# Performance work log

Hardware: AMD Instinct MI355X
Metric: run time of the kernel (lower is better)

Reference implementation:

```python
import jax, jax.numpy as jnp
import numpy as np

B, S, D = 2, 4096, 512
H, DK, DV = 8, 64, 64
LN_EPS = 1e-5
ATTN_EPS = 1e-6


def layer_norm(x, g, b):
    mu = jnp.mean(x, axis=-1, keepdims=True)
    var = jnp.var(x, axis=-1, keepdims=True)
    return (x - mu) * jax.lax.rsqrt(var + LN_EPS) * g + b


def setup_inputs() -> dict:
    key = jax.random.key(0)
    ks = jax.random.split(key, 12)
    s = 1.0 / np.sqrt(D)
    inp = {
        "Q": jax.random.normal(ks[0], (B, S, D), jnp.float32),
        "K": jax.random.normal(ks[1], (B, S, D), jnp.float32),
        "V": jax.random.normal(ks[2], (B, S, D), jnp.float32),
        "W_q": jax.random.normal(ks[3], (D, H * DK), jnp.float32) * s,
        "W_k": jax.random.normal(ks[4], (D, H * DK), jnp.float32) * s,
        "W_v": jax.random.normal(ks[5], (D, H * DV), jnp.float32) * s,
        "W_o": jax.random.normal(ks[6], (H * DV, D), jnp.float32) * s,
        "ln1_g": jnp.ones((D,), jnp.float32),
        "ln1_b": jnp.zeros((D,), jnp.float32),
        "ln2_g": jnp.ones((D,), jnp.float32),
        "ln2_b": jnp.zeros((D,), jnp.float32),
        "w1": jax.random.normal(ks[7], (4 * D, D), jnp.float32) * s,  # torch Linear: (out, in)
        "b1": jnp.zeros((4 * D,), jnp.float32),
        "w2": jax.random.normal(ks[8], (D, 4 * D), jnp.float32) * (1.0 / np.sqrt(4 * D)),
        "b2": jnp.zeros((D,), jnp.float32),
    }
    return inp


def reference(Q, K, V, W_q, W_k, W_v, W_o, ln1_g, ln1_b, ln2_g, ln2_b, w1, b1, w2, b2):
    Qn = layer_norm(Q, ln1_g, ln1_b)
    # project and split heads: [B,S,H,dk] -> [B,H,S,dk]
    q = (Qn @ W_q).reshape(B, S, H, DK).transpose(0, 2, 1, 3)
    k = (K @ W_k).reshape(B, S, H, DK).transpose(0, 2, 1, 3)
    v = (V @ W_v).reshape(B, S, H, DV).transpose(0, 2, 1, 3)
    scores = jnp.einsum("bhqd,bhkd->bhqk", q, k) / (np.sqrt(DK) + ATTN_EPS)
    attn = jax.nn.softmax(scores, axis=-1)  # same as max-subtract softmax
    ctx = jnp.einsum("bhqk,bhkd->bhqd", attn, v)
    ctx = ctx.transpose(0, 2, 1, 3).reshape(B, S, H * DV)
    att_out = ctx @ W_o  # dropout = identity (eval)
    X = Q + att_out
    Xn = layer_norm(X, ln2_g, ln2_b)
    h = jax.nn.gelu(Xn @ w1.T + b1, approximate=False)
    ffn = h @ w2.T + b2
    return X + ffn
```

## Files before the change

kernel.cpp:

```cpp
#include <hip/hip_runtime.h>

typedef unsigned short u16;
typedef __attribute__((ext_vector_type(8))) short short8;
typedef __attribute__((ext_vector_type(4))) float f32x4;
typedef __attribute__((ext_vector_type(16))) float f32x16;
typedef __attribute__((ext_vector_type(4))) unsigned u32x4;

struct __align__(8) us4 { u16 x, y, z, w; };
struct __align__(8) ui2 { unsigned x, y; };

#define CEXP (1.44269504089f / (8.0f + 1e-6f))

__device__ __forceinline__ u16 f2bf(float f) {
  unsigned u = __builtin_bit_cast(unsigned, f);
  unsigned r = (u + 0x7FFFu + ((u >> 16) & 1u)) >> 16;
  return (u16)r;
}

__device__ __forceinline__ unsigned pack_bf2_trunc(float a, float b) {
  return __builtin_amdgcn_perm(__builtin_bit_cast(unsigned, b),
                               __builtin_bit_cast(unsigned, a), 0x07060302u);
}

__device__ __forceinline__ void async_load16(const void* g, void* l) {
  __builtin_amdgcn_global_load_lds((const __attribute__((address_space(1))) void*)g,
                                   (__attribute__((address_space(3))) void*)l, 16, 0, 0);
}

__global__ void prep_weights(const float* __restrict__ Wq, const float* __restrict__ Wk,
                             const float* __restrict__ Wv, const float* __restrict__ Wo,
                             const float* __restrict__ w1, const float* __restrict__ w2,
                             u16* __restrict__ wqkvT, u16* __restrict__ woT,
                             u16* __restrict__ w1b, u16* __restrict__ w2b) {
  const int z = blockIdx.y;
  const int stride = gridDim.x * blockDim.x;
  const int i0 = blockIdx.x * blockDim.x + threadIdx.x;
  if (z < 4) {
    const float* src = z == 0 ? Wq : z == 1 ? Wk : z == 2 ? Wv : Wo;
    u16* dst = z < 3 ? wqkvT + z * 512 * 512 : woT;
    const float scale = (z == 0) ? CEXP : 1.0f;
    for (int i = i0; i < 512 * 512; i += stride) {
      int n = i >> 9, k = i & 511;
      dst[i] = f2bf(src[k * 512 + n] * scale);
    }
  } else {
    const float* src = z == 4 ? w1 : w2;
    u16* dst = z == 4 ? w1b : w2b;
    for (int i = i0; i < 2048 * 512; i += stride) dst[i] = f2bf(src[i]);
  }
}

template <bool KV>
__launch_bounds__(128)
__global__ void ln_cast(const float* __restrict__ X, const float* __restrict__ gw,
                        const float* __restrict__ bw, u16* __restrict__ Y,
                        const float* __restrict__ Kin, const float* __restrict__ Vin,
                        u16* __restrict__ Kb, u16* __restrict__ Vb) {
  const int row = blockIdx.x, t = threadIdx.x;
  const size_t base = (size_t)row * 512;
  float4 x = ((const float4*)(X + base))[t];
  float s = x.x + x.y + x.z + x.w;
  float ss = x.x * x.x + x.y * x.y + x.z * x.z + x.w * x.w;
#pragma unroll
  for (int off = 32; off > 0; off >>= 1) {
    s += __shfl_xor(s, off);
    ss += __shfl_xor(ss, off);
  }
  __shared__ float red[4];
  if ((t & 63) == 0) { red[(t >> 6) * 2] = s; red[(t >> 6) * 2 + 1] = ss; }
  __syncthreads();
  const float tot = red[0] + red[2], tss = red[1] + red[3];
  const float mu = tot * (1.0f / 512.0f);
  const float var = tss * (1.0f / 512.0f) - mu * mu;
  const float rs = rsqrtf(var + 1e-5f);
  float4 g4 = ((const float4*)gw)[t];
  float4 b4 = ((const float4*)bw)[t];
  us4 o;
  o.x = f2bf((x.x - mu) * rs * g4.x + b4.x);
  o.y = f2bf((x.y - mu) * rs * g4.y + b4.y);
  o.z = f2bf((x.z - mu) * rs * g4.z + b4.z);
  o.w = f2bf((x.w - mu) * rs * g4.w + b4.w);
  ((us4*)(Y + base))[t] = o;
  if constexpr (KV) {
    float4 k4 = ((const float4*)(Kin + base))[t];
    float4 v4 = ((const float4*)(Vin + base))[t];
    us4 ko, vo;
    ko.x = f2bf(k4.x); ko.y = f2bf(k4.y); ko.z = f2bf(k4.z); ko.w = f2bf(k4.w);
    vo.x = f2bf(v4.x); vo.y = f2bf(v4.y); vo.z = f2bf(v4.z); vo.w = f2bf(v4.w);
    ((us4*)(Kb + base))[t] = ko;
    ((us4*)(Vb + base))[t] = vo;
  }
}

__launch_bounds__(256, 3)
__global__ void gemm_qkv(const u16* __restrict__ Aq, const u16* __restrict__ Ak,
                         const u16* __restrict__ Av, const u16* __restrict__ Bt,
                         u16* __restrict__ qb, u16* __restrict__ kb, u16* __restrict__ vtb) {
  __shared__ __align__(16) u16 sA[128 * 32];
  __shared__ __align__(16) u16 sB[128 * 32];
  const int tid = threadIdx.x;
  const int wave = tid >> 6, lane = tid & 63;
  const int l15 = lane & 15, quad = lane >> 4;
  const int qsw = (quad ^ ((l15 >> 1) & 3)) * 8;
  const int m0 = blockIdx.x * 128, n0 = blockIdx.y * 128;
  const int sel = n0 >> 9;
  const u16* A = sel == 0 ? Aq : sel == 1 ? Ak : Av;
  const int wm = (wave >> 1) * 64, wn = (wave & 1) * 64;
  const int u0 = wave * 64 + lane, u1 = u0 + 256;
  const int sw0 = ((u0 & 3) ^ ((u0 >> 3) & 3)) * 8;
  const int K = 512;

  const u16* a0 = A + (size_t)(m0 + (u0 >> 2)) * K + sw0;
  const u16* a1 = A + (size_t)(m0 + (u1 >> 2)) * K + sw0;
  const u16* b0 = Bt + (size_t)(n0 + (u0 >> 2)) * K + sw0;
  const u16* b1p = Bt + (size_t)(n0 + (u1 >> 2)) * K + sw0;

  f32x4 acc[4][4] = {};
  for (int k0 = 0; k0 < K; k0 += 32) {
    async_load16(a0 + k0, &sA[wave * 512]);
    async_load16(a1 + k0, &sA[2048 + wave * 512]);
    async_load16(b0 + k0, &sB[wave * 512]);
    async_load16(b1p + k0, &sB[2048 + wave * 512]);
    __syncthreads();
    short8 af[4], bfr[4];
#pragma unroll
    for (int i = 0; i < 4; i++)
      af[i] = *(const short8*)&sA[(wm + i * 16 + l15) * 32 + qsw];
#pragma unroll
    for (int j = 0; j < 4; j++)
      bfr[j] = *(const short8*)&sB[(wn + j * 16 + l15) * 32 + qsw];
#pragma unroll
    for (int i = 0; i < 4; i++)
#pragma unroll
      for (int j = 0; j < 4; j++)
        acc[i][j] = __builtin_amdgcn_mfma_f32_16x16x32_bf16(af[i], bfr[j], acc[i][j], 0, 0, 0);
    __syncthreads();
  }

#pragma unroll
  for (int i = 0; i < 4; i++) {
#pragma unroll
    for (int j = 0; j < 4; j++) {
      const int ocol = ((n0 + wn) & 511) + j * 16 + l15;
      const int row0 = m0 + wm + i * 16 + quad * 4;
      if (sel < 2) {
        u16* C = sel == 0 ? qb : kb;
#pragma unroll
        for (int r = 0; r < 4; r++) C[(size_t)(row0 + r) * 512 + ocol] = f2bf(acc[i][j][r]);
      } else {
        const int b = row0 >> 12, s0 = row0 & 4095;
        const int hh = ocol >> 6, cc = ocol & 63;
        us4 pk;
        pk.x = f2bf(acc[i][j][0]); pk.y = f2bf(acc[i][j][1]);
        pk.z = f2bf(acc[i][j][2]); pk.w = f2bf(acc[i][j][3]);
        *(us4*)&vtb[((size_t)((b * 8 + hh) * 64 + cc) << 12) + s0] = pk;
      }
    }
  }
}

template <int EP, int TN, int LB>
__launch_bounds__(256, LB)
__global__ void gemm_bt(const u16* __restrict__ A, const u16* __restrict__ Bt,
                        int M, int N, int K, void* __restrict__ Cp,
                        const float* __restrict__ bias, const float* __restrict__ res) {
  constexpr int MI = (TN == 128) ? 4 : 2;
  __shared__ __align__(16) u16 sA[128 * 32];
  __shared__ __align__(16) u16 sB[TN * 32];
  const int tid = threadIdx.x;
  const int wave = tid >> 6, lane = tid & 63;
  const int l15 = lane & 15, quad = lane >> 4;
  const int qsw = (quad ^ ((l15 >> 1) & 3)) * 8;
  const int m0 = blockIdx.x * 128, n0 = blockIdx.y * TN;
  const int wm = (TN == 128) ? (wave >> 1) * 64 : wave * 32;
  const int wn = (TN == 128) ? (wave & 1) * 64 : 0;
  const int u0 = wave * 64 + lane, u1 = u0 + 256;
  const int sw0 = ((u0 & 3) ^ ((u0 >> 3) & 3)) * 8;

  const u16* a0 = A + (size_t)(m0 + (u0 >> 2)) * K + sw0;
  const u16* a1 = A + (size_t)(m0 + (u1 >> 2)) * K + sw0;
  const u16* b0 = Bt + (size_t)(n0 + (u0 >> 2)) * K + sw0;

  f32x4 acc[MI][4] = {};
  for (int k0 = 0; k0 < K; k0 += 32) {
    async_load16(a0 + k0, &sA[wave * 512]);
    async_load16(a1 + k0, &sA[2048 + wave * 512]);
    async_load16(b0 + k0, &sB[wave * 512]);
    if constexpr (TN == 128) {
      const u16* b1p = Bt + (size_t)(n0 + (u1 >> 2)) * K + sw0;
      async_load16(b1p + k0, &sB[2048 + wave * 512]);
    }
    __syncthreads();
    short8 af[MI], bfr[4];
#pragma unroll
    for (int i = 0; i < MI; i++)
      af[i] = *(const short8*)&sA[(wm + i * 16 + l15) * 32 + qsw];
#pragma unroll
    for (int j = 0; j < 4; j++)
      bfr[j] = *(const short8*)&sB[(wn + j * 16 + l15) * 32 + qsw];
#pragma unroll
    for (int i = 0; i < MI; i++)
#pragma unroll
      for (int j = 0; j < 4; j++)
        acc[i][j] = __builtin_amdgcn_mfma_f32_16x16x32_bf16(af[i], bfr[j], acc[i][j], 0, 0, 0);
    __syncthreads();
  }

#pragma unroll
  for (int i = 0; i < MI; i++) {
#pragma unroll
    for (int j = 0; j < 4; j++) {
      const int col = n0 + wn + j * 16 + l15;
      const int row0 = m0 + wm + i * 16 + quad * 4;
      if (EP == 2) {
        float* C = (float*)Cp;
#pragma unroll
        for (int r = 0; r < 4; r++) {
          size_t idx = (size_t)(row0 + r) * N + col;
          C[idx] = acc[i][j][r] + res[idx];
        }
      } else if (EP == 3) {
        u16* C = (u16*)Cp;
        const float bv = bias[col];
#pragma unroll
        for (int r = 0; r < 4; r++) {
          float xx = acc[i][j][r] + bv;
          float gl = 0.5f * xx * (1.0f + erff(xx * 0.70710678118f));
          C[(size_t)(row0 + r) * N + col] = f2bf(gl);
        }
      } else {
        float* C = (float*)Cp;
        const float bv = bias[col];
#pragma unroll
        for (int r = 0; r < 4; r++) {
          size_t idx = (size_t)(row0 + r) * N + col;
          C[idx] = acc[i][j][r] + bv + res[idx];
        }
      }
    }
  }
}

__launch_bounds__(512, 2)
__global__ void attn_kernel(const u16* __restrict__ qb, const u16* __restrict__ kb,
                            const u16* __restrict__ vtb, u16* __restrict__ ctx) {
  __shared__ __align__(16) u16 smem[49152];
  const int tid = threadIdx.x;
  const int wave = tid >> 6, lane = tid & 63;
  const int l31 = lane & 31, hi = lane >> 5;
  const int qg = wave & 3, kh = wave >> 2;
  const int bh = blockIdx.y, b = bh >> 3, h = bh & 7;
  const int q0 = blockIdx.x * 256;
  const size_t rb = (size_t)b * 4096;
  const int qrowA = q0 + qg * 64 + l31;
  const int qrowB = qrowA + 32;

  short8 qfA[4], qfB[4];
#pragma unroll
  for (int ks = 0; ks < 4; ks++) {
    qfA[ks] = *(const short8*)&qb[(rb + qrowA) * 512 + h * 64 + ks * 16 + hi * 8];
    qfB[ks] = *(const short8*)&qb[(rb + qrowB) * 512 + h * 64 + ks * 16 + hi * 8];
  }

  const int uk0 = wave * 64 + lane, uk1 = uk0 + 512;
  const int krow0 = uk0 >> 3, ksl0 = (uk0 & 7) ^ (krow0 & 7);
  const int krow1 = uk1 >> 3, ksl1 = (uk1 & 7) ^ (krow1 & 7);
  const u16* kp0 = kb + (rb + krow0) * 512 + h * 64 + ksl0 * 8;
  const u16* kp1 = kb + (rb + krow1) * 512 + h * 64 + ksl1 * 8;
  const int vrow0 = uk0 >> 4, vsl0 = (uk0 & 15) ^ (vrow0 & 7);
  const int vrow1 = uk1 >> 4, vsl1 = (uk1 & 15) ^ (vrow1 & 7);
  const u16* vp0 = vtb + (size_t)(bh * 64 + vrow0) * 4096 + vsl0 * 8;
  const u16* vp1 = vtb + (size_t)(bh * 64 + vrow1) * 4096 + vsl1 * 8;

#define STAGE(bi)                                                   \
  {                                                                 \
    u16* dK = smem + (bi) * 8192;                                   \
    u16* dV = smem + 24576 + (bi) * 8192;                           \
    async_load16(kp0, &dK[(wave * 64) * 8]);                        \
    async_load16(kp1, &dK[(512 + wave * 64) * 8]);                  \
    async_load16(vp0, &dV[(wave * 64) * 8]);                        \
    async_load16(vp1, &dV[(512 + wave * 64) * 8]);                  \
    kp0 += 128 * 512; kp1 += 128 * 512; vp0 += 128; vp1 += 128;     \
  }

  f32x16 ovA[2] = {}, ovB[2] = {};
  float lA = 0.f, lB = 0.f;

  STAGE(0);
  STAGE(1);
  asm volatile("s_waitcnt vmcnt(4)" ::: "memory");
  __syncthreads();

  for (int t = 0; t < 32; t++) {
    const int cur = t % 3;
    if (t < 30) STAGE((t + 2) % 3);
    const u16* K_ = smem + cur * 8192;
    const u16* V_ = smem + 24576 + cur * 8192;
#pragma unroll
    for (int kk2 = 0; kk2 < 2; kk2++) {
      const int kb32 = kh * 2 + kk2;
      f32x16 stA = {}, stB = {};
      __builtin_amdgcn_s_setprio(1);
#pragma unroll
      for (int ks = 0; ks < 4; ks++) {
        const int row = kb32 * 32 + l31;
        const int sl = (ks * 2 + hi) ^ (l31 & 7);
        short8 kf = *(const short8*)&K_[row * 64 + sl * 8];
        stA = __builtin_amdgcn_mfma_f32_32x32x16_bf16(kf, qfA[ks], stA, 0, 0, 0);
        stB = __builtin_amdgcn_mfma_f32_32x32x16_bf16(kf, qfB[ks], stB, 0, 0, 0);
      }
      __builtin_amdgcn_s_setprio(0);
      float pA[16], pB[16];
#pragma unroll
      for (int i = 0; i < 16; i++) pA[i] = __builtin_amdgcn_exp2f(stA[i]);
#pragma unroll
      for (int i = 0; i < 16; i++) pB[i] = __builtin_amdgcn_exp2f(stB[i]);
#pragma unroll
      for (int i = 0; i < 16; i += 4) {
        lA += (pA[i] + pA[i + 1]) + (pA[i + 2] + pA[i + 3]);
        lB += (pB[i] + pB[i + 1]) + (pB[i + 2] + pB[i + 3]);
      }
      unsigned a0 = pack_bf2_trunc(pA[0], pA[1]), a1 = pack_bf2_trunc(pA[2], pA[3]);
      unsigned a2 = pack_bf2_trunc(pA[4], pA[5]), a3 = pack_bf2_trunc(pA[6], pA[7]);
      unsigned a4 = pack_bf2_trunc(pA[8], pA[9]), a5 = pack_bf2_trunc(pA[10], pA[11]);
      unsigned a6 = pack_bf2_trunc(pA[12], pA[13]), a7 = pack_bf2_trunc(pA[14], pA[15]);
      auto ra0 = __builtin_amdgcn_permlane32_swap(a0, a2, false, false);
      auto ra1 = __builtin_amdgcn_permlane32_swap(a1, a3, false, false);
      auto ra2 = __builtin_amdgcn_permlane32_swap(a4, a6, false, false);
      auto ra3 = __builtin_amdgcn_permlane32_swap(a5, a7, false, false);
      u32x4 wa0 = {ra0[0], ra1[0], ra0[1], ra1[1]};
      u32x4 wa1 = {ra2[0], ra3[0], ra2[1], ra3[1]};
      short8 pfA0 = __builtin_bit_cast(short8, wa0);
      short8 pfA1 = __builtin_bit_cast(short8, wa1);
      unsigned b0 = pack_bf2_trunc(pB[0], pB[1]), b1 = pack_bf2_trunc(pB[2], pB[3]);
      unsigned b2 = pack_bf2_trunc(pB[4], pB[5]), b3 = pack_bf2_trunc(pB[6], pB[7]);
      unsigned b4 = pack_bf2_trunc(pB[8], pB[9]), b5 = pack_bf2_trunc(pB[10], pB[11]);
      unsigned b6 = pack_bf2_trunc(pB[12], pB[13]), b7 = pack_bf2_trunc(pB[14], pB[15]);
      auto rb0 = __builtin_amdgcn_permlane32_swap(b0, b2, false, false);
      auto rb1 = __builtin_amdgcn_permlane32_swap(b1, b3, false, false);
      auto rb2 = __builtin_amdgcn_permlane32_swap(b4, b6, false, false);
      auto rb3 = __builtin_amdgcn_permlane32_swap(b5, b7, false, false);
      u32x4 wb0 = {rb0[0], rb1[0], rb0[1], rb1[1]};
      u32x4 wb1 = {rb2[0], rb3[0], rb2[1], rb3[1]};
      short8 pfB0 = __builtin_bit_cast(short8, wb0);
      short8 pfB1 = __builtin_bit_cast(short8, wb1);
      __builtin_amdgcn_s_setprio(1);
#pragma unroll
      for (int vb = 0; vb < 2; vb++) {
        const int row = vb * 32 + l31;
        const int sl0 = (kb32 * 4 + hi) ^ (l31 & 7);
        const int sl1 = (kb32 * 4 + 2 + hi) ^ (l31 & 7);
        short8 vf0 = *(const short8*)&V_[row * 128 + sl0 * 8];
        short8 vf1 = *(const short8*)&V_[row * 128 + sl1 * 8];
        ovA[vb] = __builtin_amdgcn_mfma_f32_32x32x16_bf16(vf0, pfA0, ovA[vb], 0, 0, 0);
        ovA[vb] = __builtin_amdgcn_mfma_f32_32x32x16_bf16(vf1, pfA1, ovA[vb], 0, 0, 0);
        ovB[vb] = __builtin_amdgcn_mfma_f32_32x32x16_bf16(vf0, pfB0, ovB[vb], 0, 0, 0);
        ovB[vb] = __builtin_amdgcn_mfma_f32_32x32x16_bf16(vf1, pfB1, ovB[vb], 0, 0, 0);
      }
      __builtin_amdgcn_s_setprio(0);
    }
    if (t < 31) {
      if (t < 30)
        asm volatile("s_waitcnt vmcnt(4)" ::: "memory");
      else
        asm volatile("s_waitcnt vmcnt(0)" ::: "memory");
      __syncthreads();
    }
  }
#undef STAGE

  float l2A = lA + __shfl_xor(lA, 32);
  float l2B = lB + __shfl_xor(lB, 32);
  __syncthreads();
  float* mrg = (float*)&smem[0];
  float* mrgl = (float*)&smem[32768];
  if (kh == 1) {
#pragma unroll
    for (int vb = 0; vb < 2; vb++)
#pragma unroll
      for (int e = 0; e < 16; e++) {
        mrg[((qg * 2 + 0) * 32 + vb * 16 + e) * 64 + lane] = ovA[vb][e];
        mrg[((qg * 2 + 1) * 32 + vb * 16 + e) * 64 + lane] = ovB[vb][e];
      }
    mrgl[(qg * 2 + 0) * 64 + lane] = l2A;
    mrgl[(qg * 2 + 1) * 64 + lane] = l2B;
  }
  __syncthreads();
  if (kh == 0) {
    const float invA = 1.0f / (l2A + mrgl[(qg * 2 + 0) * 64 + lane]);
    const float invB = 1.0f / (l2B + mrgl[(qg * 2 + 1) * 64 + lane]);
#pragma unroll
    for (int vb = 0; vb < 2; vb++) {
#pragma unroll
      for (int rg = 0; rg < 4; rg++) {
        us4 oA, oB;
        oA.x = f2bf((ovA[vb][rg * 4 + 0] + mrg[((qg * 2 + 0) * 32 + vb * 16 + rg * 4 + 0) * 64 + lane]) * invA);
        oA.y = f2bf((ovA[vb][rg * 4 + 1] + mrg[((qg * 2 + 0) * 32 + vb * 16 + rg * 4 + 1) * 64 + lane]) * invA);
        oA.z = f2bf((ovA[vb][rg * 4 + 2] + mrg[((qg * 2 + 0) * 32 + vb * 16 + rg * 4 + 2) * 64 + lane]) * invA);
        oA.w = f2bf((ovA[vb][rg * 4 + 3] + mrg[((qg * 2 + 0) * 32 + vb * 16 + rg * 4 + 3) * 64 + lane]) * invA);
        *(us4*)&ctx[(rb + qrowA) * 512 + h * 64 + vb * 32 + rg * 8 + hi * 4] = oA;
        oB.x = f2bf((ovB[vb][rg * 4 + 0] + mrg[((qg * 2 + 1) * 32 + vb * 16 + rg * 4 + 0) * 64 + lane]) * invB);
        oB.y = f2bf((ovB[vb][rg * 4 + 1] + mrg[((qg * 2 + 1) * 32 + vb * 16 + rg * 4 + 1) * 64 + lane]) * invB);
        oB.z = f2bf((ovB[vb][rg * 4 + 2] + mrg[((qg * 2 + 1) * 32 + vb * 16 + rg * 4 + 2) * 64 + lane]) * invB);
        oB.w = f2bf((ovB[vb][rg * 4 + 3] + mrg[((qg * 2 + 1) * 32 + vb * 16 + rg * 4 + 3) * 64 + lane]) * invB);
        *(us4*)&ctx[(rb + qrowB) * 512 + h * 64 + vb * 32 + rg * 8 + hi * 4] = oB;
      }
    }
  }
}

extern "C" void kernel_launch(void* const* d_in, const int* in_sizes, int n_in,
                              void* d_out, int out_size, void* d_ws, size_t ws_size,
                              hipStream_t stream) {
  (void)in_sizes; (void)n_in; (void)out_size; (void)ws_size;
  const float* Q = (const float*)d_in[0];
  const float* K = (const float*)d_in[1];
  const float* V = (const float*)d_in[2];
  const float* W_q = (const float*)d_in[3];
  const float* W_k = (const float*)d_in[4];
  const float* W_v = (const float*)d_in[5];
  const float* W_o = (const float*)d_in[6];
  const float* ln1_g = (const float*)d_in[7];
  const float* ln1_b = (const float*)d_in[8];
  const float* ln2_g = (const float*)d_in[9];
  const float* ln2_b = (const float*)d_in[10];
  const float* w1 = (const float*)d_in[11];
  const float* b1 = (const float*)d_in[12];
  const float* w2 = (const float*)d_in[13];
  const float* b2 = (const float*)d_in[14];

  char* w = (char*)d_ws;
  const size_t MB = 1u << 20;
  u16* wqkvT = (u16*)(w);
  u16* woT = (u16*)(w + 3 * MB / 2);
  u16* w1b = (u16*)(w + 2 * MB);
  u16* w2b = (u16*)(w + 4 * MB);
  u16* Qn  = (u16*)(w + 6 * MB);
  u16* Kb  = (u16*)(w + 14 * MB);
  u16* Vb  = (u16*)(w + 22 * MB);
  u16* qb  = (u16*)(w + 30 * MB);
  u16* kb  = (u16*)(w + 38 * MB);
  u16* vtb = (u16*)(w + 46 * MB);
  u16* ctx = (u16*)(w + 54 * MB);
  float* X = (float*)(w + 62 * MB);
  u16* Xn  = (u16*)(w + 6 * MB);
  u16* hb  = (u16*)(w + 14 * MB);

  prep_weights<<<dim3(128, 6), 256, 0, stream>>>(W_q, W_k, W_v, W_o, w1, w2,
                                                 wqkvT, woT, w1b, w2b);
  ln_cast<true><<<8192, 128, 0, stream>>>(Q, ln1_g, ln1_b, Qn, K, V, Kb, Vb);
  gemm_qkv<<<dim3(64, 12), 256, 0, stream>>>(Qn, Kb, Vb, wqkvT, qb, kb, vtb);
  attn_kernel<<<dim3(16, 16), 512, 0, stream>>>(qb, kb, vtb, ctx);
  gemm_bt<2, 64, 3><<<dim3(64, 8), 256, 0, stream>>>(ctx, woT, 8192, 512, 512, X, nullptr, Q);
  ln_cast<false><<<8192, 128, 0, stream>>>(X, ln2_g, ln2_b, Xn, nullptr, nullptr, nullptr, nullptr);
  gemm_bt<3, 128, 3><<<dim3(64, 16), 256, 0, stream>>>(Xn, w1b, 8192, 2048, 512, hb, b1, nullptr);
  gemm_bt<4, 64, 3><<<dim3(64, 8), 256, 0, stream>>>(hb, w2b, 8192, 512, 2048, (float*)d_out, b2, X);
}
```

Baseline: 322.8 us.

## Split attention keys across four waves per query group and double the grid

The attention kernel now uses 128 query rows per block, with 2 query groups × 4 key-split waves instead of 4 × 2. The grid doubles to 512 blocks, with batch-head as the fast grid axis. The K/V pipeline drops from triple to double buffering, which shrinks shared memory and raises the occupancy target to 4 blocks per CU. Each wave handles one 32-key slice per tile, and a two-step shared-memory tree reduction merges the four partial outputs and sums. The goals are more parallelism and occupancy across CUs. The cost is a full vmcnt(0) wait every iteration, which exposes load latency, plus extra reduction traffic and a risk of register pressure under the tighter launch bound.

```diff
diff --git a/kernel.cpp b/kernel.cpp
--- a/kernel.cpp
+++ b/kernel.cpp
@@ -241,16 +241,16 @@
   }
 }
 
-__launch_bounds__(512, 2)
+__launch_bounds__(512, 4)
 __global__ void attn_kernel(const u16* __restrict__ qb, const u16* __restrict__ kb,
                             const u16* __restrict__ vtb, u16* __restrict__ ctx) {
-  __shared__ __align__(16) u16 smem[49152];
+  __shared__ __align__(16) u16 smem[33792];
   const int tid = threadIdx.x;
   const int wave = tid >> 6, lane = tid & 63;
   const int l31 = lane & 31, hi = lane >> 5;
-  const int qg = wave & 3, kh = wave >> 2;
-  const int bh = blockIdx.y, b = bh >> 3, h = bh & 7;
-  const int q0 = blockIdx.x * 256;
+  const int qg = wave >> 2, kh = wave & 3;
+  const int bh = blockIdx.x, b = bh >> 3, h = bh & 7;
+  const int q0 = blockIdx.y * 128;
   const size_t rb = (size_t)b * 4096;
   const int qrowA = q0 + qg * 64 + l31;
   const int qrowB = qrowA + 32;
@@ -275,7 +275,7 @@
 #define STAGE(bi)                                                   \
   {                                                                 \
     u16* dK = smem + (bi) * 8192;                                   \
-    u16* dV = smem + 24576 + (bi) * 8192;                           \
+    u16* dV = smem + 16384 + (bi) * 8192;                           \
     async_load16(kp0, &dK[(wave * 64) * 8]);                        \
     async_load16(kp1, &dK[(512 + wave * 64) * 8]);                  \
     async_load16(vp0, &dV[(wave * 64) * 8]);                        \
@@ -287,93 +287,110 @@
   float lA = 0.f, lB = 0.f;
 
   STAGE(0);
-  STAGE(1);
-  asm volatile("s_waitcnt vmcnt(4)" ::: "memory");
+  asm volatile("s_waitcnt vmcnt(0)" ::: "memory");
   __syncthreads();
 
   for (int t = 0; t < 32; t++) {
-    const int cur = t % 3;
-    if (t < 30) STAGE((t + 2) % 3);
+    const int cur = t & 1;
+    if (t < 31) STAGE(cur ^ 1);
     const u16* K_ = smem + cur * 8192;
-    const u16* V_ = smem + 24576 + cur * 8192;
-#pragma unroll
-    for (int kk2 = 0; kk2 < 2; kk2++) {
-      const int kb32 = kh * 2 + kk2;
-      f32x16 stA = {}, stB = {};
-      __builtin_amdgcn_s_setprio(1);
-#pragma unroll
-      for (int ks = 0; ks < 4; ks++) {
-        const int row = kb32 * 32 + l31;
-        const int sl = (ks * 2 + hi) ^ (l31 & 7);
-        short8 kf = *(const short8*)&K_[row * 64 + sl * 8];
-        stA = __builtin_amdgcn_mfma_f32_32x32x16_bf16(kf, qfA[ks], stA, 0, 0, 0);
-        stB = __builtin_amdgcn_mfma_f32_32x32x16_bf16(kf, qfB[ks], stB, 0, 0, 0);
-      }
-      __builtin_amdgcn_s_setprio(0);
-      float pA[16], pB[16];
-#pragma unroll
-      for (int i = 0; i < 16; i++) pA[i] = __builtin_amdgcn_exp2f(stA[i]);
-#pragma unroll
-      for (int i = 0; i < 16; i++) pB[i] = __builtin_amdgcn_exp2f(stB[i]);
-#pragma unroll
-      for (int i = 0; i < 16; i += 4) {
-        lA += (pA[i] + pA[i + 1]) + (pA[i + 2] + pA[i + 3]);
-        lB += (pB[i] + pB[i + 1]) + (pB[i + 2] + pB[i + 3]);
-      }
-      unsigned a0 = pack_bf2_trunc(pA[0], pA[1]), a1 = pack_bf2_trunc(pA[2], pA[3]);
-      unsigned a2 = pack_bf2_trunc(pA[4], pA[5]), a3 = pack_bf2_trunc(pA[6], pA[7]);
-      unsigned a4 = pack_bf2_trunc(pA[8], pA[9]), a5 = pack_bf2_trunc(pA[10], pA[11]);
-      unsigned a6 = pack_bf2_trunc(pA[12], pA[13]), a7 = pack_bf2_trunc(pA[14], pA[15]);
-      auto ra0 = __builtin_amdgcn_permlane32_swap(a0, a2, false, false);
-      auto ra1 = __builtin_amdgcn_permlane32_swap(a1, a3, false, false);
-      auto ra2 = __builtin_amdgcn_permlane32_swap(a4, a6, false, false);
-      auto ra3 = __builtin_amdgcn_permlane32_swap(a5, a7, false, false);
-      u32x4 wa0 = {ra0[0], ra1[0], ra0[1], ra1[1]};
-      u32x4 wa1 = {ra2[0], ra3[0], ra2[1], ra3[1]};
-      short8 pfA0 = __builtin_bit_cast(short8, wa0);
-      short8 pfA1 = __builtin_bit_cast(short8, wa1);
-      unsigned b0 = pack_bf2_trunc(pB[0], pB[1]), b1 = pack_bf2_trunc(pB[2], pB[3]);
-      unsigned b2 = pack_bf2_trunc(pB[4], pB[5]), b3 = pack_bf2_trunc(pB[6], pB[7]);
-      unsigned b4 = pack_bf2_trunc(pB[8], pB[9]), b5 = pack_bf2_trunc(pB[10], pB[11]);
-      unsigned b6 = pack_bf2_trunc(pB[12], pB[13]), b7 = pack_bf2_trunc(pB[14], pB[15]);
-      auto rb0 = __builtin_amdgcn_permlane32_swap(b0, b2, false, false);
-      auto rb1 = __builtin_amdgcn_permlane32_swap(b1, b3, false, false);
-      auto rb2 = __builtin_amdgcn_permlane32_swap(b4, b6, false, false);
-      auto rb3 = __builtin_amdgcn_permlane32_swap(b5, b7, false, false);
-      u32x4 wb0 = {rb0[0], rb1[0], rb0[1], rb1[1]};
-      u32x4 wb1 = {rb2[0], rb3[0], rb2[1], rb3[1]};
-      short8 pfB0 = __builtin_bit_cast(short8, wb0);
-      short8 pfB1 = __builtin_bit_cast(short8, wb1);
-      __builtin_amdgcn_s_setprio(1);
-#pragma unroll
-      for (int vb = 0; vb < 2; vb++) {
-        const int row = vb * 32 + l31;
-        const int sl0 = (kb32 * 4 + hi) ^ (l31 & 7);
-        const int sl1 = (kb32 * 4 + 2 + hi) ^ (l31 & 7);
-        short8 vf0 = *(const short8*)&V_[row * 128 + sl0 * 8];
-        short8 vf1 = *(const short8*)&V_[row * 128 + sl1 * 8];
-        ovA[vb] = __builtin_amdgcn_mfma_f32_32x32x16_bf16(vf0, pfA0, ovA[vb], 0, 0, 0);
-        ovA[vb] = __builtin_amdgcn_mfma_f32_32x32x16_bf16(vf1, pfA1, ovA[vb], 0, 0, 0);
-        ovB[vb] = __builtin_amdgcn_mfma_f32_32x32x16_bf16(vf0, pfB0, ovB[vb], 0, 0, 0);
-        ovB[vb] = __builtin_amdgcn_mfma_f32_32x32x16_bf16(vf1, pfB1, ovB[vb], 0, 0, 0);
-      }
-      __builtin_amdgcn_s_setprio(0);
-    }
-    if (t < 31) {
-      if (t < 30)
-        asm volatile("s_waitcnt vmcnt(4)" ::: "memory");
-      else
-        asm volatile("s_waitcnt vmcnt(0)" ::: "memory");
-      __syncthreads();
-    }
+    const u16* V_ = smem + 16384 + cur * 8192;
+    f32x16 stA = {}, stB = {};
+    __builtin_amdgcn_s_setprio(1);
+#pragma unroll
+    for (int ks = 0; ks < 4; ks++) {
+      const int row = kh * 32 + l31;
+      const int sl = (ks * 2 + hi) ^ (l31 & 7);
+      short8 kf = *(const short8*)&K_[row * 64 + sl * 8];
+      stA = __builtin_amdgcn_mfma_f32_32x32x16_bf16(kf, qfA[ks], stA, 0, 0, 0);
+      stB = __builtin_amdgcn_mfma_f32_32x32x16_bf16(kf, qfB[ks], stB, 0, 0, 0);
+    }
+    __builtin_amdgcn_s_setprio(0);
+    float pA[16], pB[16];
+#pragma unroll
+    for (int i = 0; i < 16; i++) pA[i] = __builtin_amdgcn_exp2f(stA[i]);
+#pragma unroll
+    for (int i = 0; i < 16; i++) pB[i] = __builtin_amdgcn_exp2f(stB[i]);
+#pragma unroll
+    for (int i = 0; i < 16; i += 4) {
+      lA += (pA[i] + pA[i + 1]) + (pA[i + 2] + pA[i + 3]);
+      lB += (pB[i] + pB[i + 1]) + (pB[i + 2] + pB[i + 3]);
+    }
+    unsigned a0 = pack_bf2_trunc(pA[0], pA[1]), a1 = pack_bf2_trunc(pA[2], pA[3]);
+    unsigned a2 = pack_bf2_trunc(pA[4], pA[5]), a3 = pack_bf2_trunc(pA[6], pA[7]);
+    unsigned a4 = pack_bf2_trunc(pA[8], pA[9]), a5 = pack_bf2_trunc(pA[10], pA[11]);
+    unsigned a6 = pack_bf2_trunc(pA[12], pA[13]), a7 = pack_bf2_trunc(pA[14], pA[15]);
+    auto ra0 = __builtin_amdgcn_permlane32_swap(a0, a2, false, false);
+    auto ra1 = __builtin_amdgcn_permlane32_swap(a1, a3, false, false);
+    auto ra2 = __builtin_amdgcn_permlane32_swap(a4, a6, false, false);
+    auto ra3 = __builtin_amdgcn_permlane32_swap(a5, a7, false, false);
+    u32x4 wa0 = {ra0[0], ra1[0], ra0[1], ra1[1]};
+    u32x4 wa1 = {ra2[0], ra3[0], ra2[1], ra3[1]};
+    short8 pfA0 = __builtin_bit_cast(short8, wa0);
+    short8 pfA1 = __builtin_bit_cast(short8, wa1);
+    unsigned b0 = pack_bf2_trunc(pB[0], pB[1]), b1 = pack_bf2_trunc(pB[2], pB[3]);
+    unsigned b2 = pack_bf2_trunc(pB[4], pB[5]), b3 = pack_bf2_trunc(pB[6], pB[7]);
+    unsigned b4 = pack_bf2_trunc(pB[8], pB[9]), b5 = pack_bf2_trunc(pB[10], pB[11]);
+    unsigned b6 = pack_bf2_trunc(pB[12], pB[13]), b7 = pack_bf2_trunc(pB[14], pB[15]);
+    auto rb0 = __builtin_amdgcn_permlane32_swap(b0, b2, false, false);
+    auto rb1 = __builtin_amdgcn_permlane32_swap(b1, b3, false, false);
+    auto rb2 = __builtin_amdgcn_permlane32_swap(b4, b6, false, false);
+    auto rb3 = __builtin_amdgcn_permlane32_swap(b5, b7, false, false);
+    u32x4 wb0 = {rb0[0], rb1[0], rb0[1], rb1[1]};
+    u32x4 wb1 = {rb2[0], rb3[0], rb2[1], rb3[1]};
+    short8 pfB0 = __builtin_bit_cast(short8, wb0);
+    short8 pfB1 = __builtin_bit_cast(short8, wb1);
+    __builtin_amdgcn_s_setprio(1);
+#pragma unroll
+    for (int vb = 0; vb < 2; vb++) {
+      const int row = vb * 32 + l31;
+      const int sl0 = (kh * 4 + hi) ^ (l31 & 7);
+      const int sl1 = (kh * 4 + 2 + hi) ^ (l31 & 7);
+      short8 vf0 = *(const short8*)&V_[row * 128 + sl0 * 8];
+      short8 vf1 = *(const short8*)&V_[row * 128 + sl1 * 8];
+      ovA[vb] = __builtin_amdgcn_mfma_f32_32x32x16_bf16(vf0, pfA0, ovA[vb], 0, 0, 0);
+      ovA[vb] = __builtin_amdgcn_mfma_f32_32x32x16_bf16(vf1, pfA1, ovA[vb], 0, 0, 0);
+      ovB[vb] = __builtin_amdgcn_mfma_f32_32x32x16_bf16(vf0, pfB0, ovB[vb], 0, 0, 0);
+      ovB[vb] = __builtin_amdgcn_mfma_f32_32x32x16_bf16(vf1, pfB1, ovB[vb], 0, 0, 0);
+    }
+    __builtin_amdgcn_s_setprio(0);
+    asm volatile("s_waitcnt vmcnt(0)" ::: "memory");
+    __syncthreads();
   }
 #undef STAGE
 
   float l2A = lA + __shfl_xor(lA, 32);
   float l2B = lB + __shfl_xor(lB, 32);
+  float* mrg = (float*)smem;
+  float* mrgl = (float*)smem + 16384;
+  if (kh >= 2) {
+    float* r = mrg + (kh - 2) * 8192;
+    float* rl = mrgl + (kh - 2) * 256;
+#pragma unroll
+    for (int vb = 0; vb < 2; vb++)
+#pragma unroll
+      for (int e = 0; e < 16; e++) {
+        r[((qg * 2 + 0) * 32 + vb * 16 + e) * 64 + lane] = ovA[vb][e];
+        r[((qg * 2 + 1) * 32 + vb * 16 + e) * 64 + lane] = ovB[vb][e];
+      }
+    rl[(qg * 2 + 0) * 64 + lane] = l2A;
+    rl[(qg * 2 + 1) * 64 + lane] = l2B;
+  }
   __syncthreads();
-  float* mrg = (float*)&smem[0];
-  float* mrgl = (float*)&smem[32768];
+  if (kh < 2) {
+    float* r = mrg + kh * 8192;
+    float* rl = mrgl + kh * 256;
+#pragma unroll
+    for (int vb = 0; vb < 2; vb++)
+#pragma unroll
+      for (int e = 0; e < 16; e++) {
+        ovA[vb][e] += r[((qg * 2 + 0) * 32 + vb * 16 + e) * 64 + lane];
+        ovB[vb][e] += r[((qg * 2 + 1) * 32 + vb * 16 + e) * 64 + lane];
+      }
+    l2A += rl[(qg * 2 + 0) * 64 + lane];
+    l2B += rl[(qg * 2 + 1) * 64 + lane];
+  }
+  __syncthreads();
   if (kh == 1) {
 #pragma unroll
     for (int vb = 0; vb < 2; vb++)
@@ -450,7 +467,7 @@
                                                  wqkvT, woT, w1b, w2b);
   ln_cast<true><<<8192, 128, 0, stream>>>(Q, ln1_g, ln1_b, Qn, K, V, Kb, Vb);
   gemm_qkv<<<dim3(64, 12), 256, 0, stream>>>(Qn, Kb, Vb, wqkvT, qb, kb, vtb);
-  attn_kernel<<<dim3(16, 16), 512, 0, stream>>>(qb, kb, vtb, ctx);
+  attn_kernel<<<dim3(16, 32), 512, 0, stream>>>(qb, kb, vtb, ctx);
   gemm_bt<2, 64, 3><<<dim3(64, 8), 256, 0, stream>>>(ctx, woT, 8192, 512, 512, X, nullptr, Q);
   ln_cast<false><<<8192, 128, 0, stream>>>(X, ln2_g, ln2_b, Xn, nullptr, nullptr, nullptr, nullptr);
   gemm_bt<3, 128, 3><<<dim3(64, 16), 256, 0, stream>>>(Xn, w1b, 8192, 2048, 512, hb, b1, nullptr);
```

Result: slower. 430.6 us (+33.4%).
